# Performance work log

Measured on AMD Instinct MI355X. Metric: run time of the kernel, lower is better.

The kernel has to match this reference:

```python
import jax, jax.numpy as jnp
import numpy as np

BETA = 0.25  # commitment cost (original code's undefined self.betas)


def setup_inputs() -> dict:
    key = jax.random.key(0)
    k1, k2 = jax.random.split(key)
    B, D, H, W = 32, 256, 32, 32
    K = 1024
    x = jax.random.normal(k1, (B, D, H, W), dtype=jnp.float32)
    # nn.Embedding init: uniform(-1/K, 1/K)
    emb = jax.random.uniform(k2, (K, D), dtype=jnp.float32,
                             minval=-1.0 / K, maxval=1.0 / K)
    return {"x": x, "emb": emb}


def reference(x, emb):
    # x: [B, D, H, W] -> NHWC
    xp = jnp.transpose(x, (0, 2, 3, 1))          # [B, H, W, D]
    D = emb.shape[1]
    z = xp.reshape(-1, D)                        # [N, D]
    # pairwise squared distance: ||z||^2 + ||e||^2 - 2 z e^T
    dist = (jnp.sum(z * z, axis=1, keepdims=True)
            + jnp.sum(emb * emb, axis=1)
            - 2.0 * jnp.einsum('nd,kd->nk', z, emb))  # [N, K]
    idx = jnp.argmin(dist, axis=1)               # [N] int
    z_quant = emb[idx].reshape(xp.shape)         # [B, H, W, D]
    sg = jax.lax.stop_gradient
    loss = (jnp.mean((sg(z_quant) - xp) ** 2)
            + BETA * jnp.mean((z_quant - sg(xp)) ** 2))
    # straight-through estimator
    z_quant = xp + sg(z_quant - xp)
    z_quant = jnp.transpose(z_quant, (0, 3, 1, 2))  # back to NCHW
    return z_quant, idx, loss
```

## Files before the change

kernel.cpp:

```cpp
#include <hip/hip_runtime.h>

typedef _Float16 half8 __attribute__((ext_vector_type(8)));
typedef _Float16 half4v __attribute__((ext_vector_type(4)));
typedef float f32x4 __attribute__((ext_vector_type(4)));

#define ZQ_ELEMS 8388608
#define N_TOK    32768
#define D_DIM    256
#define K_CB     1024

#define FLAG_CAP 32768
#define ESCALE   1024.0f
#define TAU      0.15f

__device__ __align__(16) _Float16 g_eh[K_CB * D_DIM];
__device__ __align__(16) float g_ebT[D_DIM * K_CB];
__device__ float g_ck[K_CB];
__device__ float g_bk[K_CB];
__device__ float g_loss;
__device__ int   g_cnt;
__device__ int   g_flags[FLAG_CAP];

__global__ __launch_bounds__(256) void vq_prep(const float* __restrict__ emb) {
  const int tid = threadIdx.x;
  const int w   = tid >> 6;
  const int l   = tid & 63;
  const int k   = (blockIdx.x << 2) + w;
  f32x4 v = *(const f32x4*)(emb + (k << 8) + (l << 2));
  double sd = (double)v[0]*v[0] + (double)v[1]*v[1] + (double)v[2]*v[2] + (double)v[3]*v[3];
  #pragma unroll
  for (int m = 1; m < 64; m <<= 1) sd += __shfl_xor(sd, m);
  if (l == 0) { g_bk[k] = (float)sd; g_ck[k] = 512.0f * (float)sd; }
  half4v h;
  h[0] = (_Float16)(v[0] * ESCALE); h[1] = (_Float16)(v[1] * ESCALE);
  h[2] = (_Float16)(v[2] * ESCALE); h[3] = (_Float16)(v[3] * ESCALE);
  *(half4v*)(g_eh + (k << 8) + (l << 2)) = h;
  if (blockIdx.x == 0 && tid == 0) { g_loss = 0.0f; g_cnt = 0; }
}

__global__ __launch_bounds__(256) void vq_tr(const float* __restrict__ emb) {
  __shared__ float tl[64][65];
  const int tx = threadIdx.x & 63, ty = threadIdx.x >> 6;
  const int k0 = (blockIdx.x & 15) << 6;
  const int d0 = (blockIdx.x >> 4) << 6;
  #pragma unroll
  for (int j = 0; j < 16; j++) {
    const int kk = (ty << 4) + j;
    tl[kk][tx] = emb[((k0 + kk) << 8) + d0 + tx];
  }
  __syncthreads();
  #pragma unroll
  for (int j = 0; j < 16; j++) {
    const int dd = (ty << 4) + j;
    g_ebT[((d0 + dd) << 10) + k0 + tx] = tl[tx][dd];
  }
}

__global__ __launch_bounds__(256, 2) void vq_main(const float* __restrict__ x,
                                                  const float* __restrict__ emb,
                                                  float* __restrict__ out) {
  __shared__ __align__(16) _Float16 zt[64 * 256];
  __shared__ float ckl[K_CB];
  __shared__ float wv1[4][64], wv2[4][64];
  __shared__ int   wi1[4][64];
  __shared__ int   fidx[64];
  __shared__ float lred[4];

  const int tid = threadIdx.x;
  const int n0  = blockIdx.x * 64;
  const int b   = blockIdx.x >> 4;
  const int hw0 = (blockIdx.x & 15) << 6;

  #pragma unroll
  for (int i = 0; i < 4; i++) ckl[tid + 256 * i] = g_ck[tid + 256 * i];

  {
    const int hw8 = (tid & 7) << 3;
    const int dl  = tid >> 3;
    #pragma unroll
    for (int it = 0; it < 8; it++) {
      const int d = (it << 5) + dl;
      const float* src = x + (((b << 8) + d) << 10) + hw0 + hw8;
      f32x4 a0 = *(const f32x4*)src;
      f32x4 a1 = *(const f32x4*)(src + 4);
      _Float16 cv[8];
      cv[0]=(_Float16)a0[0]; cv[1]=(_Float16)a0[1]; cv[2]=(_Float16)a0[2]; cv[3]=(_Float16)a0[3];
      cv[4]=(_Float16)a1[0]; cv[5]=(_Float16)a1[1]; cv[6]=(_Float16)a1[2]; cv[7]=(_Float16)a1[3];
      const int blkx = d >> 3;
      #pragma unroll
      for (int i = 0; i < 8; i++) {
        const int n   = hw8 + i;
        const int blk = blkx ^ i ^ (tid & 7);
        zt[(n << 8) + (blk << 3) + (d & 7)] = cv[i];
      }
    }
  }
  __syncthreads();

  const int w = tid >> 6;
  const int l = tid & 63;
  const int c = l & 15;
  const int q = l >> 4;

  half8 af[4][8];
  #pragma unroll
  for (int t = 0; t < 4; t++) {
    const int n  = (t << 4) + c;
    const int sw = (n & 7) ^ (n >> 3);
    #pragma unroll
    for (int s = 0; s < 8; s++) {
      const int K = (s << 2) + q;
      af[t][s] = *(const half8*)(zt + (n << 8) + ((K ^ sw) << 3));
    }
  }

  float v1[4][4], v2[4][4]; int i1[4][4];
  #pragma unroll
  for (int t = 0; t < 4; t++)
    #pragma unroll
    for (int r = 0; r < 4; r++) { v1[t][r] = -3e38f; v2[t][r] = -3e38f; i1[t][r] = 0; }

  for (int jj = 0; jj < 16; jj++) {
    const int k0 = (w << 4) + (jj << 6);
    const float ckv = ckl[k0 + c];
    f32x4 acc[4];
    #pragma unroll
    for (int t = 0; t < 4; t++) acc[t] = f32x4{-ckv, -ckv, -ckv, -ckv};
    #pragma unroll
    for (int s = 0; s < 8; s++) {
      const half8 bf = *(const half8*)(g_eh + ((k0 + c) << 8) + (s << 5) + (q << 3));
      #pragma unroll
      for (int t = 0; t < 4; t++)
        acc[t] = __builtin_amdgcn_mfma_f32_16x16x32_f16(af[t][s], bf, acc[t], 0, 0, 0);
    }
    const int kk = k0 + c;
    #pragma unroll
    for (int t = 0; t < 4; t++)
      #pragma unroll
      for (int r = 0; r < 4; r++) {
        const float sv = acc[t][r];
        if (sv > v1[t][r]) { v2[t][r] = v1[t][r]; v1[t][r] = sv; i1[t][r] = kk; }
        else if (sv > v2[t][r]) v2[t][r] = sv;
      }
  }

  #pragma unroll
  for (int t = 0; t < 4; t++)
    #pragma unroll
    for (int r = 0; r < 4; r++) {
      float a1v = v1[t][r], a2v = v2[t][r]; int ai = i1[t][r];
      #pragma unroll
      for (int m = 8; m >= 1; m >>= 1) {
        const float o1 = __shfl_xor(a1v, m);
        const int   oi = __shfl_xor(ai, m);
        const float o2 = __shfl_xor(a2v, m);
        if (o1 > a1v || (o1 == a1v && oi < ai)) { a2v = fmaxf(a1v, o2); a1v = o1; ai = oi; }
        else a2v = fmaxf(a2v, o1);
      }
      if (c == 0) {
        const int nl = (t << 4) + (q << 2) + r;
        wv1[w][nl] = a1v; wv2[w][nl] = a2v; wi1[w][nl] = ai;
      }
    }
  __syncthreads();

  if (tid < 64) {
    float a1v = wv1[0][tid], a2v = wv2[0][tid]; int ai = wi1[0][tid];
    #pragma unroll
    for (int ww = 1; ww < 4; ww++) {
      const float o1 = wv1[ww][tid]; const int oi = wi1[ww][tid]; const float o2 = wv2[ww][tid];
      if (o1 > a1v || (o1 == a1v && oi < ai)) { a2v = fmaxf(a1v, o2); a1v = o1; ai = oi; }
      else a2v = fmaxf(a2v, o1);
    }
    fidx[tid] = ai;
    out[ZQ_ELEMS + n0 + tid] = (float)ai;
    if (a1v - a2v < TAU) {
      int p = atomicAdd(&g_cnt, 1);
      if (p < FLAG_CAP) g_flags[p] = n0 + tid;
    }
  }
  __syncthreads();

  float lacc = 0.0f;
  {
    const int hw = tid & 63;
    const int sw = (hw & 7) ^ (hw >> 3);
    const float* erow = emb + (fidx[hw] << 8);
    #pragma unroll
    for (int it = 0; it < 8; it++) {
      const int dblk = (it << 2) + w;
      half8 zv = *(const half8*)(zt + (hw << 8) + ((dblk ^ sw) << 3));
      f32x4 e0 = *(const f32x4*)(erow + (dblk << 3));
      f32x4 e1 = *(const f32x4*)(erow + (dblk << 3) + 4);
      #pragma unroll
      for (int j = 0; j < 8; j++) {
        const int d = (dblk << 3) + j;
        const float ef = (j < 4) ? e0[j] : e1[j - 4];
        const float df = ef - (float)zv[j];
        lacc += df * df;
        out[(((b << 8) + d) << 10) + hw0 + hw] = ef;
      }
    }
  }
  #pragma unroll
  for (int m = 1; m < 64; m <<= 1) lacc += __shfl_xor(lacc, m);
  if (l == 0) lred[w] = lacc;
  __syncthreads();
  if (tid == 0) atomicAdd(&g_loss, lred[0] + lred[1] + lred[2] + lred[3]);
}

__global__ __launch_bounds__(256) void vq_fix(const float* __restrict__ x,
                                              float* __restrict__ out) {
  __shared__ float zt2[2][256];
  __shared__ float aA2[2];
  __shared__ float bvv[2][256];
  __shared__ int   bkk[2][256];
  __shared__ int   nn[2];
  const int tid = threadIdx.x;
  int cnt = g_cnt; if (cnt > FLAG_CAP) cnt = FLAG_CAP;
  const int ngrp = (cnt + 1) >> 1;
  for (int grp = blockIdx.x; grp < ngrp; grp += gridDim.x) {
    const int n0 = grp << 1;
    if (tid < 2) nn[tid] = g_flags[(n0 + tid < cnt) ? (n0 + tid) : (cnt - 1)];
    __syncthreads();
    #pragma unroll
    for (int g = 0; g < 2; g++) {
      const int n = nn[g], b = n >> 10, hw = n & 1023;
      zt2[g][tid] = x[(((b << 8) + tid) << 10) + hw];
    }
    __syncthreads();
    if (tid < 128 && (tid & 63) < 32) {
      const int g = tid >> 6, l32 = tid & 31;
      double sa = 0.0;
      #pragma unroll
      for (int j = 0; j < 8; j++) { const double z = (double)zt2[g][(l32 << 3) + j]; sa += z * z; }
      #pragma unroll
      for (int m = 1; m < 32; m <<= 1) sa += __shfl_xor(sa, m);
      if (l32 == 0) aA2[g] = (float)sa;
    }
    __syncthreads();
    double c0[4] = {0.0, 0.0, 0.0, 0.0};
    double c1[4] = {0.0, 0.0, 0.0, 0.0};
    #pragma unroll 4
    for (int d = 0; d < 256; d++) {
      const float* col = g_ebT + (d << 10);
      const double z0 = (double)zt2[0][d];
      const double z1 = (double)zt2[1][d];
      #pragma unroll
      for (int r = 0; r < 4; r++) {
        const double e = (double)col[(r << 8) + tid];
        c0[r] = fma(e, z0, c0[r]);
        c1[r] = fma(e, z1, c1[r]);
      }
    }
    const float A0 = aA2[0], A1 = aA2[1];
    float bv0 = 3.4e38f, bv1 = 3.4e38f; int bk0 = 0, bk1 = 0;
    #pragma unroll
    for (int r = 0; r < 4; r++) {
      const int k = (r << 8) + tid;
      const float bkv = g_bk[k];
      const float D0 = (A0 + bkv) - 2.0f * (float)c0[r];
      const float D1 = (A1 + bkv) - 2.0f * (float)c1[r];
      if (D0 < bv0) { bv0 = D0; bk0 = k; }
      if (D1 < bv1) { bv1 = D1; bk1 = k; }
    }
    bvv[0][tid] = bv0; bkk[0][tid] = bk0;
    bvv[1][tid] = bv1; bkk[1][tid] = bk1;
    __syncthreads();
    for (int off = 128; off >= 1; off >>= 1) {
      if (tid < off) {
        #pragma unroll
        for (int g = 0; g < 2; g++) {
          const float v2c = bvv[g][tid + off]; const int k2 = bkk[g][tid + off];
          if (v2c < bvv[g][tid] || (v2c == bvv[g][tid] && k2 < bkk[g][tid])) {
            bvv[g][tid] = v2c; bkk[g][tid] = k2;
          }
        }
      }
      __syncthreads();
    }
    if (tid < 2 && n0 + tid < cnt) out[ZQ_ELEMS + nn[tid]] = (float)bkk[tid][0];
    __syncthreads();
  }
}

__global__ void vq_fin(float* __restrict__ out) {
  out[ZQ_ELEMS + N_TOK] = g_loss * (1.25f / 8388608.0f);
}

extern "C" void kernel_launch(void* const* d_in, const int* in_sizes, int n_in,
                              void* d_out, int out_size, void* d_ws, size_t ws_size,
                              hipStream_t stream) {
  const float* x   = (const float*)d_in[0];
  const float* emb = (const float*)d_in[1];
  float* out = (float*)d_out;
  vq_prep<<<256, 256, 0, stream>>>(emb);
  vq_tr<<<64, 256, 0, stream>>>(emb);
  vq_main<<<512, 256, 0, stream>>>(x, emb, out);
  vq_fix<<<512, 256, 0, stream>>>(x, out);
  vq_fin<<<1, 1, 0, stream>>>(out);
}
```

Measured before the change: 202.7 us.

## Split VQ fix-up pass into staged tokens and codebook-quarter jobs with atomicMin merge

The fallback exact-distance pass for flagged tokens now stages each flagged token's vector and squared norm into global buffers. It then splits every token pair across four independent codebook-quarter jobs, so four times as many blocks run. Partial argmins are merged with a 64-bit atomicMin on an order-preserving key that packs distance and index, and a final small kernel writes the indices. The flag capacity also drops from 32768 to 8192, which risks silently dropping flagged tokens if more than 8192 are flagged. It also adds two extra kernel launches and more global traffic.

```diff
diff --git a/kernel.cpp b/kernel.cpp
--- a/kernel.cpp
+++ b/kernel.cpp
@@ -9,7 +9,7 @@
 #define D_DIM    256
 #define K_CB     1024
 
-#define FLAG_CAP 32768
+#define FLAG_CAP 8192
 #define ESCALE   1024.0f
 #define TAU      0.15f
 
@@ -20,6 +20,15 @@
 __device__ float g_loss;
 __device__ int   g_cnt;
 __device__ int   g_flags[FLAG_CAP];
+__device__ float g_zst[FLAG_CAP * 256];
+__device__ float g_aA[FLAG_CAP];
+__device__ unsigned long long g_best[FLAG_CAP];
+
+__device__ __forceinline__ unsigned long long enc_dk(float D, int k) {
+  unsigned int b = __float_as_uint(D);
+  unsigned int u = (b & 0x80000000u) ? ~b : (b | 0x80000000u);
+  return (((unsigned long long)u) << 32) | (unsigned int)k;
+}
 
 __global__ __launch_bounds__(256) void vq_prep(const float* __restrict__ emb) {
   const int tid = threadIdx.x;
@@ -35,6 +44,8 @@
   h[0] = (_Float16)(v[0] * ESCALE); h[1] = (_Float16)(v[1] * ESCALE);
   h[2] = (_Float16)(v[2] * ESCALE); h[3] = (_Float16)(v[3] * ESCALE);
   *(half4v*)(g_eh + (k << 8) + (l << 2)) = h;
+  const int gi = blockIdx.x * 256 + tid;
+  if (gi < FLAG_CAP) g_best[gi] = ~0ULL;
   if (blockIdx.x == 0 && tid == 0) { g_loss = 0.0f; g_cnt = 0; }
 }
 
@@ -209,63 +220,56 @@
   if (tid == 0) atomicAdd(&g_loss, lred[0] + lred[1] + lred[2] + lred[3]);
 }
 
-__global__ __launch_bounds__(256) void vq_fix(const float* __restrict__ x,
-                                              float* __restrict__ out) {
-  __shared__ float zt2[2][256];
-  __shared__ float aA2[2];
+__global__ __launch_bounds__(256) void vq_stage(const float* __restrict__ x) {
+  __shared__ float zl[256];
+  const int tid = threadIdx.x;
+  int cnt = g_cnt; if (cnt > FLAG_CAP) cnt = FLAG_CAP;
+  for (int s = blockIdx.x; s < cnt; s += gridDim.x) {
+    const int n = g_flags[s], b = n >> 10, hw = n & 1023;
+    const float zv = x[(((b << 8) + tid) << 10) + hw];
+    g_zst[(s << 8) + tid] = zv;
+    zl[tid] = zv;
+    __syncthreads();
+    if (tid < 32) {
+      double sa = 0.0;
+      #pragma unroll
+      for (int j = 0; j < 8; j++) { const double z = (double)zl[(tid << 3) + j]; sa += z * z; }
+      #pragma unroll
+      for (int m = 1; m < 32; m <<= 1) sa += __shfl_xor(sa, m);
+      if (tid == 0) g_aA[s] = (float)sa;
+    }
+    __syncthreads();
+  }
+}
+
+__global__ __launch_bounds__(256) void vq_fix() {
+  __shared__ float z0l[256], z1l[256];
   __shared__ float bvv[2][256];
   __shared__ int   bkk[2][256];
-  __shared__ int   nn[2];
   const int tid = threadIdx.x;
   int cnt = g_cnt; if (cnt > FLAG_CAP) cnt = FLAG_CAP;
-  const int ngrp = (cnt + 1) >> 1;
-  for (int grp = blockIdx.x; grp < ngrp; grp += gridDim.x) {
-    const int n0 = grp << 1;
-    if (tid < 2) nn[tid] = g_flags[(n0 + tid < cnt) ? (n0 + tid) : (cnt - 1)];
-    __syncthreads();
-    #pragma unroll
-    for (int g = 0; g < 2; g++) {
-      const int n = nn[g], b = n >> 10, hw = n & 1023;
-      zt2[g][tid] = x[(((b << 8) + tid) << 10) + hw];
-    }
-    __syncthreads();
-    if (tid < 128 && (tid & 63) < 32) {
-      const int g = tid >> 6, l32 = tid & 31;
-      double sa = 0.0;
-      #pragma unroll
-      for (int j = 0; j < 8; j++) { const double z = (double)zt2[g][(l32 << 3) + j]; sa += z * z; }
-      #pragma unroll
-      for (int m = 1; m < 32; m <<= 1) sa += __shfl_xor(sa, m);
-      if (l32 == 0) aA2[g] = (float)sa;
-    }
-    __syncthreads();
-    double c0[4] = {0.0, 0.0, 0.0, 0.0};
-    double c1[4] = {0.0, 0.0, 0.0, 0.0};
-    #pragma unroll 4
+  const int njob = ((cnt + 1) >> 1) << 2;
+  for (int j = blockIdx.x; j < njob; j += gridDim.x) {
+    const int pr = j >> 2, r = j & 3;
+    const int s0 = pr << 1;
+    const int s1 = (s0 + 1 < cnt) ? s0 + 1 : cnt - 1;
+    z0l[tid] = g_zst[(s0 << 8) + tid];
+    z1l[tid] = g_zst[(s1 << 8) + tid];
+    __syncthreads();
+    double c0 = 0.0, c1 = 0.0;
+    const float* colbase = g_ebT + (r << 8) + tid;
+    #pragma unroll 8
     for (int d = 0; d < 256; d++) {
-      const float* col = g_ebT + (d << 10);
-      const double z0 = (double)zt2[0][d];
-      const double z1 = (double)zt2[1][d];
-      #pragma unroll
-      for (int r = 0; r < 4; r++) {
-        const double e = (double)col[(r << 8) + tid];
-        c0[r] = fma(e, z0, c0[r]);
-        c1[r] = fma(e, z1, c1[r]);
-      }
-    }
-    const float A0 = aA2[0], A1 = aA2[1];
-    float bv0 = 3.4e38f, bv1 = 3.4e38f; int bk0 = 0, bk1 = 0;
-    #pragma unroll
-    for (int r = 0; r < 4; r++) {
-      const int k = (r << 8) + tid;
-      const float bkv = g_bk[k];
-      const float D0 = (A0 + bkv) - 2.0f * (float)c0[r];
-      const float D1 = (A1 + bkv) - 2.0f * (float)c1[r];
-      if (D0 < bv0) { bv0 = D0; bk0 = k; }
-      if (D1 < bv1) { bv1 = D1; bk1 = k; }
-    }
-    bvv[0][tid] = bv0; bkk[0][tid] = bk0;
-    bvv[1][tid] = bv1; bkk[1][tid] = bk1;
+      const double e = (double)colbase[d << 10];
+      c0 = fma(e, (double)z0l[d], c0);
+      c1 = fma(e, (double)z1l[d], c1);
+    }
+    const int k = (r << 8) + tid;
+    const float bkv = g_bk[k];
+    bvv[0][tid] = (g_aA[s0] + bkv) - 2.0f * (float)c0;
+    bkk[0][tid] = k;
+    bvv[1][tid] = (g_aA[s1] + bkv) - 2.0f * (float)c1;
+    bkk[1][tid] = k;
     __syncthreads();
     for (int off = 128; off >= 1; off >>= 1) {
       if (tid < off) {
@@ -279,9 +283,18 @@
       }
       __syncthreads();
     }
-    if (tid < 2 && n0 + tid < cnt) out[ZQ_ELEMS + nn[tid]] = (float)bkk[tid][0];
-    __syncthreads();
-  }
+    if (tid == 0) {
+      atomicMin(&g_best[s0], enc_dk(bvv[0][0], bkk[0][0]));
+      atomicMin(&g_best[s1], enc_dk(bvv[1][0], bkk[1][0]));
+    }
+    __syncthreads();
+  }
+}
+
+__global__ __launch_bounds__(256) void vq_out(float* __restrict__ out) {
+  int cnt = g_cnt; if (cnt > FLAG_CAP) cnt = FLAG_CAP;
+  for (int s = blockIdx.x * 256 + threadIdx.x; s < cnt; s += gridDim.x * 256)
+    out[ZQ_ELEMS + g_flags[s]] = (float)(unsigned int)(g_best[s] & 0xFFFFFFFFu);
 }
 
 __global__ void vq_fin(float* __restrict__ out) {
@@ -297,6 +310,8 @@
   vq_prep<<<256, 256, 0, stream>>>(emb);
   vq_tr<<<64, 256, 0, stream>>>(emb);
   vq_main<<<512, 256, 0, stream>>>(x, emb, out);
-  vq_fix<<<512, 256, 0, stream>>>(x, out);
+  vq_stage<<<1024, 256, 0, stream>>>(x);
+  vq_fix<<<2048, 256, 0, stream>>>();
+  vq_out<<<32, 256, 0, stream>>>(out);
   vq_fin<<<1, 1, 0, stream>>>(out);
 }
```

After: 198.3 us. -2.2%, faster.
